# Optimization experiments

Measured on AMD Instinct MI355X. Metric: run time of the kernel, lower is better.

The kernel has to match this reference:

```python
import jax, jax.numpy as jnp
import numpy as np

N = 200000   # nodes per branch
E = 600000   # directed edges per branch
G = 8192     # graphs per batch
F_IN = 7
H = 128
OUT = 2
BN_EPS = 1e-5


def setup_inputs() -> dict:
    key = jax.random.key(0)
    ks = jax.random.split(key, 16)
    s = 0.05
    inp = {
        "x_c": jax.random.normal(ks[0], (N, F_IN), jnp.float32),
        "edge_index_c": jax.random.randint(ks[1], (2, E), 0, N, jnp.int32),
        "batch_c": jnp.sort(jax.random.randint(ks[2], (N,), 0, G, jnp.int32)),
        "x_s": jax.random.normal(ks[3], (N, F_IN), jnp.float32),
        "edge_index_s": jax.random.randint(ks[4], (2, E), 0, N, jnp.int32),
        "batch_s": jnp.sort(jax.random.randint(ks[5], (N,), 0, G, jnp.int32)),
        "Wc0": jax.random.normal(ks[6], (F_IN, H), jnp.float32) * s,
        "bc0": jnp.zeros((H,), jnp.float32),
        "Wc1": jax.random.normal(ks[7], (H, H), jnp.float32) * s,
        "bc1": jnp.zeros((H,), jnp.float32),
        "bnc_gamma": jnp.ones((2, H), jnp.float32),
        "bnc_beta": jnp.zeros((2, H), jnp.float32),
        "bnc_mean": jax.random.normal(ks[8], (2, H), jnp.float32) * 0.01,
        "bnc_var": jnp.ones((2, H), jnp.float32),
        "Ws0": jax.random.normal(ks[9], (F_IN, H), jnp.float32) * s,
        "bs0": jnp.zeros((H,), jnp.float32),
        "Ws1": jax.random.normal(ks[10], (H, H), jnp.float32) * s,
        "bs1": jnp.zeros((H,), jnp.float32),
        "bns_gamma": jnp.ones((2, H), jnp.float32),
        "bns_beta": jnp.zeros((2, H), jnp.float32),
        "bns_mean": jax.random.normal(ks[11], (2, H), jnp.float32) * 0.01,
        "bns_var": jnp.ones((2, H), jnp.float32),
        "fc1_w": jax.random.normal(ks[12], (2 * H, H), jnp.float32) * s,
        "fc1_b": jnp.zeros((H,), jnp.float32),
        "fc2_w": jax.random.normal(ks[13], (H, OUT), jnp.float32) * s,
        "fc2_b": jnp.zeros((OUT,), jnp.float32),
        "num_graphs": G,
    }
    return inp


def _gcn_conv(x, src, dst, W, b):
    """PyG GCNConv: D^{-1/2}(A+I)D^{-1/2} X W + b, self-loops added."""
    n = x.shape[0]
    h = x @ W                                   # [n, H]
    loop = jnp.arange(n, dtype=src.dtype)
    src2 = jnp.concatenate([src, loop])
    dst2 = jnp.concatenate([dst, loop])
    deg = jax.ops.segment_sum(jnp.ones_like(dst2, h.dtype), dst2, num_segments=n)
    dinv = jnp.where(deg > 0, jax.lax.rsqrt(deg), 0.0)
    coef = (dinv[src2] * dinv[dst2])[:, None]   # [E+n, 1]
    out = jax.ops.segment_sum(h[src2] * coef, dst2, num_segments=n)
    return out + b


def _branch(x, ei, W0, b0, W1, b1, gamma, beta, mean, var):
    src, dst = ei[0], ei[1]
    for i, (W, b) in enumerate(((W0, b0), (W1, b1))):
        x = _gcn_conv(x, src, dst, W, b)
        # BatchNorm1d (eval mode) + ReLU; dropout is identity in eval
        x = (x - mean[i]) * jax.lax.rsqrt(var[i] + BN_EPS) * gamma[i] + beta[i]
        x = jax.nn.relu(x)
    return x


def _mean_pool(x, batch, num_graphs):
    s = jax.ops.segment_sum(x, batch, num_segments=num_graphs)
    cnt = jax.ops.segment_sum(jnp.ones_like(batch, x.dtype), batch, num_segments=num_graphs)
    return s / jnp.maximum(cnt, 1.0)[:, None]


def reference(x_c, edge_index_c, batch_c, x_s, edge_index_s, batch_s,
              Wc0, bc0, Wc1, bc1, bnc_gamma, bnc_beta, bnc_mean, bnc_var,
              Ws0, bs0, Ws1, bs1, bns_gamma, bns_beta, bns_mean, bns_var,
              fc1_w, fc1_b, fc2_w, fc2_b, num_graphs):
    hc = _branch(x_c, edge_index_c, Wc0, bc0, Wc1, bc1,
                 bnc_gamma, bnc_beta, bnc_mean, bnc_var)
    hs = _branch(x_s, edge_index_s, Ws0, bs0, Ws1, bs1,
                 bns_gamma, bns_beta, bns_mean, bns_var)
    pc = _mean_pool(hc, batch_c, num_graphs)   # [G, H]
    ps = _mean_pool(hs, batch_s, num_graphs)   # [G, H]
    x = jnp.concatenate([pc, ps], axis=1)      # [G, 2H]
    x = jax.nn.relu(x @ fc1_w + fc1_b)
    return x @ fc2_w + fc2_b                   # [G, 2]
```

## Files before the change

### kernel.cpp

```cpp
#include <hip/hip_runtime.h>

#define NN 200000
#define NE 600000
#define NG 8192
#define HD 128
#define FIN 7
#define BN_EPS 1e-5f

#define CHUNK 1024
#define NB 196
#define TA 64
#define NPG 8
#define NBT (NN / TA)
#define ECAP 320
#define GMAX 8

__global__ void k_hist(const int* __restrict__ dstC, const int* __restrict__ dstS,
                       const int* __restrict__ batchC, const int* __restrict__ batchS,
                       int* __restrict__ degC, int* __restrict__ degS,
                       int* __restrict__ cntC, int* __restrict__ cntS) {
    int e = blockIdx.x * 256 + threadIdx.x;
    if (e < NE)            atomicAdd(&degC[dstC[e]], 1);
    else if (e < 2 * NE)   atomicAdd(&degS[dstS[e - NE]], 1);
    if (e < NN)                      atomicAdd(&cntC[batchC[e]], 1);
    else if (e >= NE && e < NE + NN) atomicAdd(&cntS[batchS[e - NE]], 1);
}

__global__ void k_scan1m(const int* __restrict__ degC, const int* __restrict__ degS,
                         int* __restrict__ bsumC, int* __restrict__ bsumS,
                         float* __restrict__ dinvC, float* __restrict__ dinvS,
                         const float* __restrict__ xC, const float* __restrict__ xS,
                         float* __restrict__ xsC, float* __restrict__ xsS) {
    __shared__ int sd[256];
    int t = threadIdx.x;
    int b = blockIdx.x;
    bool sBr = b >= NB;
    int bb = sBr ? b - NB : b;
    const int* deg = sBr ? degS : degC;
    const float* x = sBr ? xS : xC;
    float* dinv = sBr ? dinvS : dinvC;
    float* xs   = sBr ? xsS : xsC;
    int* bsum = sBr ? bsumS : bsumC;
    int base = bb * CHUNK + t * 4;
    int s = 0;
#pragma unroll
    for (int j = 0; j < 4; j++) {
        int i = base + j;
        if (i < NN) {
            int d = deg[i];
            s += d;
            float di = rsqrtf((float)(d + 1));
            dinv[i] = di;
            float4 v0, v1;
            v0.x = x[(size_t)i * FIN + 0] * di;
            v0.y = x[(size_t)i * FIN + 1] * di;
            v0.z = x[(size_t)i * FIN + 2] * di;
            v0.w = x[(size_t)i * FIN + 3] * di;
            v1.x = x[(size_t)i * FIN + 4] * di;
            v1.y = x[(size_t)i * FIN + 5] * di;
            v1.z = x[(size_t)i * FIN + 6] * di;
            v1.w = 0.f;
            *reinterpret_cast<float4*>(&xs[(size_t)i * 8])     = v0;
            *reinterpret_cast<float4*>(&xs[(size_t)i * 8 + 4]) = v1;
        }
    }
    sd[t] = s; __syncthreads();
    for (int st = 128; st > 0; st >>= 1) { if (t < st) sd[t] += sd[t + st]; __syncthreads(); }
    if (t == 0) bsum[bb] = sd[0];
}

__global__ void k_scan2m(int* __restrict__ bsumC, int* __restrict__ bsumS) {
    __shared__ int sd[256];
    int* bsum = blockIdx.x ? bsumS : bsumC;
    int t = threadIdx.x;
    int v = (t < NB) ? bsum[t] : 0;
    sd[t] = v; __syncthreads();
    for (int st = 1; st < 256; st <<= 1) {
        int add = (t >= st) ? sd[t - st] : 0;
        __syncthreads();
        sd[t] += add;
        __syncthreads();
    }
    if (t < NB) bsum[t] = sd[t] - v;
}

__global__ void k_scan3m(const int* __restrict__ degC, const int* __restrict__ degS,
                         const int* __restrict__ bsumC, const int* __restrict__ bsumS,
                         int* __restrict__ offsC, int* __restrict__ offsS,
                         int* __restrict__ curC, int* __restrict__ curS) {
    __shared__ int sd[256];
    int t = threadIdx.x;
    int b = blockIdx.x;
    bool sBr = b >= NB;
    int bb = sBr ? b - NB : b;
    const int* deg  = sBr ? degS  : degC;
    const int* bsum = sBr ? bsumS : bsumC;
    int* offs   = sBr ? offsS : offsC;
    int* cursor = sBr ? curS  : curC;
    int base = bb * CHUNK + t * 4;
    int v[4]; int s = 0;
#pragma unroll
    for (int j = 0; j < 4; j++) { int i = base + j; v[j] = (i < NN) ? deg[i] : 0; s += v[j]; }
    sd[t] = s; __syncthreads();
    for (int st = 1; st < 256; st <<= 1) {
        int add = (t >= st) ? sd[t - st] : 0;
        __syncthreads();
        sd[t] += add;
        __syncthreads();
    }
    int run = bsum[bb] + sd[t] - s;
#pragma unroll
    for (int j = 0; j < 4; j++) {
        int i = base + j;
        if (i < NN) { offs[i] = run; cursor[i] = run; run += v[j]; }
    }
    if (bb == 0 && t == 0) offs[NN] = NE;
}

__global__ void k_fillm(const int* __restrict__ srcC, const int* __restrict__ dstC,
                        const int* __restrict__ srcS, const int* __restrict__ dstS,
                        int* __restrict__ curC, int* __restrict__ curS,
                        int* __restrict__ csrC, int* __restrict__ csrS) {
    int e = blockIdx.x * 256 + threadIdx.x;
    if (e < NE) {
        int d = dstC[e];
        int pos = atomicAdd(&curC[d], 1);
        csrC[pos] = srcC[e];
    } else if (e < 2 * NE) {
        int ee = e - NE;
        int d = dstS[ee];
        int pos = atomicAdd(&curS[d], 1);
        csrS[pos] = srcS[ee];
    }
}

__global__ void k_aggxm(const float* __restrict__ xsC, const float* __restrict__ xsS,
                        const float* __restrict__ dinvC, const float* __restrict__ dinvS,
                        const int* __restrict__ offsC, const int* __restrict__ offsS,
                        const int* __restrict__ csrC, const int* __restrict__ csrS,
                        float* __restrict__ axdC, float* __restrict__ axdS) {
    int gid = blockIdx.x * 256 + threadIdx.x;
    bool sBr = gid >= NN * 8;
    int lid = sBr ? gid - NN * 8 : gid;
    const float* xs   = sBr ? xsS   : xsC;
    const float* dinv = sBr ? dinvS : dinvC;
    const int*   offs = sBr ? offsS : offsC;
    const int*   csr  = sBr ? csrS  : csrC;
    float*       axd  = sBr ? axdS  : axdC;
    int i = lid >> 3, f = lid & 7;
    float v = xs[lid];
    int o1 = offs[i], o2 = offs[i + 1];
    int j = o1;
    for (; j + 2 <= o2; j += 2) {
        int s0 = csr[j], s1 = csr[j + 1];
        float u0 = xs[(size_t)s0 * 8 + f];
        float u1 = xs[(size_t)s1 * 8 + f];
        v += u0; v += u1;
    }
    if (j < o2) v += xs[(size_t)csr[j] * 8 + f];
    float di = dinv[i];
    axd[lid] = (f == 7) ? di : v * di;
}

__device__ __forceinline__ void src_contrib(float4 r0, float4 r1,
                                            const float4* wp, const float4 c4, float4& a) {
    float axr[7] = { r0.x, r0.y, r0.z, r0.w, r1.x, r1.y, r1.z };
    float4 y = c4;
#pragma unroll
    for (int k = 0; k < FIN; k++) {
        y.x = fmaf(axr[k], wp[k].x, y.x);
        y.y = fmaf(axr[k], wp[k].y, y.y);
        y.z = fmaf(axr[k], wp[k].z, y.z);
        y.w = fmaf(axr[k], wp[k].w, y.w);
    }
    a.x = fmaf(fmaxf(y.x, 0.f), r1.w, a.x);
    a.y = fmaf(fmaxf(y.y, 0.f), r1.w, a.y);
    a.z = fmaf(fmaxf(y.z, 0.f), r1.w, a.z);
    a.w = fmaf(fmaxf(y.w, 0.f), r1.w, a.w);
}

#define PHASE1(GETIDX)                                                                     \
    _Pragma("unroll")                                                                      \
    for (int n = 0; n < NPG; n++) {                                                        \
        int ln = n0 + n;                                                                   \
        float4 a = make_float4(0.f, 0.f, 0.f, 0.f);                                        \
        int e = soffs[ln], ee = soffs[ln + 1];                                             \
        float4 p0 = *reinterpret_cast<const float4*>(&axd[(size_t)(nbase + ln) * 8]);      \
        float4 p1 = *reinterpret_cast<const float4*>(&axd[(size_t)(nbase + ln) * 8 + 4]);  \
        sdvN[n] = p1.w;                                                                    \
        for (; e < ee; e++) {                                                              \
            int s = (GETIDX);                                                              \
            float4 q0 = *reinterpret_cast<const float4*>(&axd[(size_t)s * 8]);             \
            float4 q1 = *reinterpret_cast<const float4*>(&axd[(size_t)s * 8 + 4]);         \
            src_contrib(p0, p1, wp, c4, a);                                                \
            p0 = q0; p1 = q1;                                                              \
        }                                                                                  \
        src_contrib(p0, p1, wp, c4, a);                                                    \
        *reinterpret_cast<float4*>(&g2[ln][f4]) = a;                                       \
    }

__global__ __launch_bounds__(256, 4) void k_agp2(
    const float* __restrict__ axdC, const float* __restrict__ axdS,
    const int* __restrict__ offsC, const int* __restrict__ offsS,
    const int* __restrict__ csrC, const int* __restrict__ csrS,
    const int* __restrict__ batchC, const int* __restrict__ batchS,
    const float* __restrict__ Wc0, const float* __restrict__ bc0,
    const float* __restrict__ bncG, const float* __restrict__ bncB,
    const float* __restrict__ bncM, const float* __restrict__ bncV,
    const float* __restrict__ Wc1, const float* __restrict__ bc1,
    const float* __restrict__ Ws0, const float* __restrict__ bs0,
    const float* __restrict__ bnsG, const float* __restrict__ bnsB,
    const float* __restrict__ bnsM, const float* __restrict__ bnsV,
    const float* __restrict__ Ws1, const float* __restrict__ bs1,
    float* __restrict__ poolC, float* __restrict__ poolS)
{
    __shared__ float g2[TA][HD];
    __shared__ float spool[GMAX * HD];
    __shared__ int soffs[TA + 1];
    __shared__ int scsr[ECAP];
    int b = blockIdx.x;
    bool sBr = b >= NBT;
    int bb = sBr ? b - NBT : b;
    const float* axd  = sBr ? axdS  : axdC;
    const int*  offs  = sBr ? offsS : offsC;
    const int*  csr   = sBr ? csrS  : csrC;
    const int*  batch = sBr ? batchS : batchC;
    const float* W0   = sBr ? Ws0 : Wc0;
    const float* b0   = sBr ? bs0 : bc0;
    const float* bnG  = sBr ? bnsG : bncG;
    const float* bnB  = sBr ? bnsB : bncB;
    const float* bnM  = sBr ? bnsM : bncM;
    const float* bnV  = sBr ? bnsV : bncV;
    const float* W1   = sBr ? Ws1 : Wc1;
    const float* b1   = sBr ? bs1 : bc1;
    float* pool       = sBr ? poolS : poolC;

    int t = threadIdx.x;
    int nbase = bb * TA;
    if (t <= TA) soffs[t] = offs[nbase + t];
#pragma unroll
    for (int r = 0; r < GMAX * HD / 256; r++) spool[r * 256 + t] = 0.f;
    __syncthreads();
    int E0 = soffs[0], E1 = soffs[TA];
    int Et = E1 - E0;
    int ecap = Et < ECAP ? Et : ECAP;
    for (int j = t; j < ecap; j += 256) scsr[j] = csr[E0 + j];

    int q = t & 31, ng = t >> 5;
    int f4 = q * 4, n0 = ng * NPG;

    float4 gm = *reinterpret_cast<const float4*>(&bnG[f4]);
    float4 vr = *reinterpret_cast<const float4*>(&bnV[f4]);
    float4 mn = *reinterpret_cast<const float4*>(&bnM[f4]);
    float4 bt = *reinterpret_cast<const float4*>(&bnB[f4]);
    float4 bb0 = *reinterpret_cast<const float4*>(&b0[f4]);
    float4 gsc;
    gsc.x = gm.x * rsqrtf(vr.x + BN_EPS);
    gsc.y = gm.y * rsqrtf(vr.y + BN_EPS);
    gsc.z = gm.z * rsqrtf(vr.z + BN_EPS);
    gsc.w = gm.w * rsqrtf(vr.w + BN_EPS);
    float4 wp[FIN];
#pragma unroll
    for (int k = 0; k < FIN; k++) {
        float4 w = *reinterpret_cast<const float4*>(&W0[k * HD + f4]);
        wp[k] = make_float4(w.x * gsc.x, w.y * gsc.y, w.z * gsc.z, w.w * gsc.w);
    }
    float4 c4 = make_float4((bb0.x - mn.x) * gsc.x + bt.x,
                            (bb0.y - mn.y) * gsc.y + bt.y,
                            (bb0.z - mn.z) * gsc.z + bt.z,
                            (bb0.w - mn.w) * gsc.w + bt.w);
    __syncthreads();

    float sdvN[NPG];
    if (Et <= ECAP) {
        PHASE1(scsr[e - E0])
    } else {
        PHASE1(((e - E0) < ECAP) ? scsr[e - E0] : csr[e])
    }
    __syncthreads();

    float acc[NPG][4];
#pragma unroll
    for (int a = 0; a < NPG; a++)
#pragma unroll
        for (int c = 0; c < 4; c++) acc[a][c] = 0.f;

    for (int k = 0; k < 128; k += 4) {
        float ha[NPG][4];
#pragma unroll
        for (int a = 0; a < NPG; a++) {
            float4 hv = *reinterpret_cast<const float4*>(&g2[n0 + a][k]);
            ha[a][0] = hv.x; ha[a][1] = hv.y; ha[a][2] = hv.z; ha[a][3] = hv.w;
        }
#pragma unroll
        for (int j = 0; j < 4; j++) {
            float4 w = *reinterpret_cast<const float4*>(&W1[(k + j) * HD + f4]);
#pragma unroll
            for (int a = 0; a < NPG; a++) {
                acc[a][0] = fmaf(ha[a][j], w.x, acc[a][0]);
                acc[a][1] = fmaf(ha[a][j], w.y, acc[a][1]);
                acc[a][2] = fmaf(ha[a][j], w.z, acc[a][2]);
                acc[a][3] = fmaf(ha[a][j], w.w, acc[a][3]);
            }
        }
    }

    float4 gm2 = *reinterpret_cast<const float4*>(&bnG[HD + f4]);
    float4 bt2 = *reinterpret_cast<const float4*>(&bnB[HD + f4]);
    float4 mn2 = *reinterpret_cast<const float4*>(&bnM[HD + f4]);
    float4 vr2 = *reinterpret_cast<const float4*>(&bnV[HD + f4]);
    float4 bb1 = *reinterpret_cast<const float4*>(&b1[f4]);
    float Ax = gm2.x * rsqrtf(vr2.x + BN_EPS), Bx = (bb1.x - mn2.x) * Ax + bt2.x;
    float Ay = gm2.y * rsqrtf(vr2.y + BN_EPS), By = (bb1.y - mn2.y) * Ay + bt2.y;
    float Az = gm2.z * rsqrtf(vr2.z + BN_EPS), Bz = (bb1.z - mn2.z) * Az + bt2.z;
    float Aw = gm2.w * rsqrtf(vr2.w + BN_EPS), Bw = (bb1.w - mn2.w) * Aw + bt2.w;

    int gfirst = batch[nbase];
    float sx = 0, sy = 0, sz = 0, sw = 0;
    int curg = -1;
#pragma unroll
    for (int a = 0; a < NPG; a++) {
        int i = nbase + n0 + a;
        int g = batch[i];
        float sdv = sdvN[a];
        float zx = fmaxf(fmaf(acc[a][0] * sdv, Ax, Bx), 0.f);
        float zy = fmaxf(fmaf(acc[a][1] * sdv, Ay, By), 0.f);
        float zz = fmaxf(fmaf(acc[a][2] * sdv, Az, Bz), 0.f);
        float zw = fmaxf(fmaf(acc[a][3] * sdv, Aw, Bw), 0.f);
        if (g != curg) {
            if (curg >= 0) {
                int slot = curg - gfirst;
                if (slot < GMAX) {
                    atomicAdd(&spool[slot * HD + f4 + 0], sx);
                    atomicAdd(&spool[slot * HD + f4 + 1], sy);
                    atomicAdd(&spool[slot * HD + f4 + 2], sz);
                    atomicAdd(&spool[slot * HD + f4 + 3], sw);
                } else {
                    atomicAdd(&pool[(size_t)curg * HD + f4 + 0], sx);
                    atomicAdd(&pool[(size_t)curg * HD + f4 + 1], sy);
                    atomicAdd(&pool[(size_t)curg * HD + f4 + 2], sz);
                    atomicAdd(&pool[(size_t)curg * HD + f4 + 3], sw);
                }
            }
            curg = g; sx = zx; sy = zy; sz = zz; sw = zw;
        } else { sx += zx; sy += zy; sz += zz; sw += zw; }
    }
    {
        int slot = curg - gfirst;
        if (slot < GMAX) {
            atomicAdd(&spool[slot * HD + f4 + 0], sx);
            atomicAdd(&spool[slot * HD + f4 + 1], sy);
            atomicAdd(&spool[slot * HD + f4 + 2], sz);
            atomicAdd(&spool[slot * HD + f4 + 3], sw);
        } else {
            atomicAdd(&pool[(size_t)curg * HD + f4 + 0], sx);
            atomicAdd(&pool[(size_t)curg * HD + f4 + 1], sy);
            atomicAdd(&pool[(size_t)curg * HD + f4 + 2], sz);
            atomicAdd(&pool[(size_t)curg * HD + f4 + 3], sw);
        }
    }
    __syncthreads();

    int glast = batch[nbase + TA - 1];
    int nslots = glast - gfirst + 1;
    if (nslots > GMAX) nslots = GMAX;
    for (int idx = t; idx < (nslots << 7); idx += 256) {
        atomicAdd(&pool[(size_t)(gfirst + (idx >> 7)) * HD + (idx & 127)], spool[idx]);
    }
}

#define GPB 8
__global__ __launch_bounds__(128) void k_mlp(
    const float* __restrict__ pc, const float* __restrict__ ps,
    const int* __restrict__ cc, const int* __restrict__ cs,
    const float* __restrict__ w1, const float* __restrict__ b1,
    const float* __restrict__ w2, const float* __restrict__ b2,
    float* __restrict__ outp)
{
    __shared__ float xc[GPB][256];
    __shared__ float hb[GPB][128];
    int t = threadIdx.x;
    int g0 = blockIdx.x * GPB;
#pragma unroll
    for (int gg = 0; gg < GPB; gg++) {
        int g = g0 + gg;
        xc[gg][t]       = pc[g * HD + t] / fmaxf((float)cc[g], 1.f);
        xc[gg][128 + t] = ps[g * HD + t] / fmaxf((float)cs[g], 1.f);
    }
    __syncthreads();
    float acc[GPB];
#pragma unroll
    for (int gg = 0; gg < GPB; gg++) acc[gg] = b1[t];
#pragma unroll 2
    for (int k = 0; k < 256; k++) {
        float w = w1[k * HD + t];
#pragma unroll
        for (int gg = 0; gg < GPB; gg++) acc[gg] = fmaf(xc[gg][k], w, acc[gg]);
    }
#pragma unroll
    for (int gg = 0; gg < GPB; gg++) hb[gg][t] = fmaxf(acc[gg], 0.f);
    __syncthreads();
    if (t < GPB * 2) {
        int gg = t >> 1, o = t & 1;
        float v = b2[o];
        for (int k = 0; k < 128; k++) v = fmaf(hb[gg][k], w2[k * 2 + o], v);
        outp[(size_t)(g0 + gg) * 2 + o] = v;
    }
}

extern "C" void kernel_launch(void* const* d_in, const int* in_sizes, int n_in,
                              void* d_out, int out_size, void* d_ws, size_t ws_size,
                              hipStream_t stream) {
    const float* x_c      = (const float*)d_in[0];
    const int*   ei_c     = (const int*)  d_in[1];
    const int*   batch_c  = (const int*)  d_in[2];
    const float* x_s      = (const float*)d_in[3];
    const int*   ei_s     = (const int*)  d_in[4];
    const int*   batch_s  = (const int*)  d_in[5];
    const float* Wc0      = (const float*)d_in[6];
    const float* bc0      = (const float*)d_in[7];
    const float* Wc1      = (const float*)d_in[8];
    const float* bc1      = (const float*)d_in[9];
    const float* bnc_g    = (const float*)d_in[10];
    const float* bnc_b    = (const float*)d_in[11];
    const float* bnc_m    = (const float*)d_in[12];
    const float* bnc_v    = (const float*)d_in[13];
    const float* Ws0      = (const float*)d_in[14];
    const float* bs0      = (const float*)d_in[15];
    const float* Ws1      = (const float*)d_in[16];
    const float* bs1      = (const float*)d_in[17];
    const float* bns_g    = (const float*)d_in[18];
    const float* bns_b    = (const float*)d_in[19];
    const float* bns_m    = (const float*)d_in[20];
    const float* bns_v    = (const float*)d_in[21];
    const float* fc1_w    = (const float*)d_in[22];
    const float* fc1_b    = (const float*)d_in[23];
    const float* fc2_w    = (const float*)d_in[24];
    const float* fc2_b    = (const float*)d_in[25];

    char* p = (char*)d_ws;
    auto take = [&](size_t bytes) {
        void* r = (void*)p;
        p += (bytes + 255) & ~(size_t)255;
        return r;
    };
    float* xs_c   = (float*)take((size_t)NN * 8 * 4);
    float* xs_s   = (float*)take((size_t)NN * 8 * 4);
    float* axd_c  = (float*)take((size_t)NN * 8 * 4);
    float* axd_s  = (float*)take((size_t)NN * 8 * 4);
    int*   deg_c  = (int*)  take((size_t)NN * 4);
    int*   deg_s  = (int*)  take((size_t)NN * 4);
    float* dinv_c = (float*)take((size_t)NN * 4);
    float* dinv_s = (float*)take((size_t)NN * 4);
    int*   offs_c = (int*)  take((size_t)(NN + 1) * 4);
    int*   offs_s = (int*)  take((size_t)(NN + 1) * 4);
    int*   cur_c  = (int*)  take((size_t)NN * 4);
    int*   cur_s  = (int*)  take((size_t)NN * 4);
    int*   csr_c  = (int*)  take((size_t)NE * 4);
    int*   csr_s  = (int*)  take((size_t)NE * 4);
    int*   bsum_c = (int*)  take((size_t)NB * 4);
    int*   bsum_s = (int*)  take((size_t)NB * 4);
    float* pool_c = (float*)take((size_t)NG * HD * 4);
    float* pool_s = (float*)take((size_t)NG * HD * 4);
    int*   cnt_c  = (int*)  take((size_t)NG * 4);
    int*   cnt_s  = (int*)  take((size_t)NG * 4);
    (void)ws_size; (void)in_sizes; (void)n_in; (void)out_size;

    hipMemsetAsync(deg_c, 0, (size_t)2 * NN * 4, stream);
    hipMemsetAsync(pool_c, 0, ((size_t)2 * NG * HD + 2 * NG) * 4, stream);

    const int* src_c = ei_c;           const int* dst_c = ei_c + NE;
    const int* src_s = ei_s;           const int* dst_s = ei_s + NE;

    k_hist  <<<(2 * NE + 255) / 256, 256, 0, stream>>>(dst_c, dst_s, batch_c, batch_s,
                                                       deg_c, deg_s, cnt_c, cnt_s);
    k_scan1m<<<2 * NB, 256, 0, stream>>>(deg_c, deg_s, bsum_c, bsum_s, dinv_c, dinv_s,
                                         x_c, x_s, xs_c, xs_s);
    k_scan2m<<<2, 256, 0, stream>>>(bsum_c, bsum_s);
    k_scan3m<<<2 * NB, 256, 0, stream>>>(deg_c, deg_s, bsum_c, bsum_s,
                                         offs_c, offs_s, cur_c, cur_s);
    k_fillm <<<(2 * NE + 255) / 256, 256, 0, stream>>>(src_c, dst_c, src_s, dst_s,
                                                       cur_c, cur_s, csr_c, csr_s);
    k_aggxm <<<2 * NN * 8 / 256, 256, 0, stream>>>(xs_c, xs_s, dinv_c, dinv_s,
                                                   offs_c, offs_s, csr_c, csr_s, axd_c, axd_s);

    k_agp2<<<2 * NBT, 256, 0, stream>>>(axd_c, axd_s,
                                        offs_c, offs_s, csr_c, csr_s, batch_c, batch_s,
                                        Wc0, bc0, bnc_g, bnc_b, bnc_m, bnc_v, Wc1, bc1,
                                        Ws0, bs0, bns_g, bns_b, bns_m, bns_v, Ws1, bs1,
                                        pool_c, pool_s);

    k_mlp<<<NG / GPB, 128, 0, stream>>>(pool_c, pool_s, cnt_c, cnt_s,
                                        fc1_w, fc1_b, fc2_w, fc2_b, (float*)d_out);
}
```

Baseline: 508.4 us.

## Record per-edge rank in histogram to drop fill atomics and fuse scan stage

The histogram kernel now saves the return value of its degree atomic as a per-edge rank. The fill kernel then places each edge at offs[dst]+rank with no atomics and no cursor array. The block-sum scan kernel is removed, and every scan3 block redundantly scans the 196 block sums in shared memory, saving one launch. In exchange it adds two 600K-int rank arrays that are written and read back, and extra per-block scan work.

```diff
diff --git a/kernel.cpp b/kernel.cpp
--- a/kernel.cpp
+++ b/kernel.cpp
@@ -18,10 +18,11 @@
 __global__ void k_hist(const int* __restrict__ dstC, const int* __restrict__ dstS,
                        const int* __restrict__ batchC, const int* __restrict__ batchS,
                        int* __restrict__ degC, int* __restrict__ degS,
-                       int* __restrict__ cntC, int* __restrict__ cntS) {
+                       int* __restrict__ cntC, int* __restrict__ cntS,
+                       int* __restrict__ rankC, int* __restrict__ rankS) {
     int e = blockIdx.x * 256 + threadIdx.x;
-    if (e < NE)            atomicAdd(&degC[dstC[e]], 1);
-    else if (e < 2 * NE)   atomicAdd(&degS[dstS[e - NE]], 1);
+    if (e < NE)            rankC[e] = atomicAdd(&degC[dstC[e]], 1);
+    else if (e < 2 * NE)   rankS[e - NE] = atomicAdd(&degS[dstS[e - NE]], 1);
     if (e < NN)                      atomicAdd(&cntC[batchC[e]], 1);
     else if (e >= NE && e < NE + NN) atomicAdd(&cntS[batchS[e - NE]], 1);
 }
@@ -69,26 +70,11 @@
     if (t == 0) bsum[bb] = sd[0];
 }
 
-__global__ void k_scan2m(int* __restrict__ bsumC, int* __restrict__ bsumS) {
-    __shared__ int sd[256];
-    int* bsum = blockIdx.x ? bsumS : bsumC;
-    int t = threadIdx.x;
-    int v = (t < NB) ? bsum[t] : 0;
-    sd[t] = v; __syncthreads();
-    for (int st = 1; st < 256; st <<= 1) {
-        int add = (t >= st) ? sd[t - st] : 0;
-        __syncthreads();
-        sd[t] += add;
-        __syncthreads();
-    }
-    if (t < NB) bsum[t] = sd[t] - v;
-}
-
 __global__ void k_scan3m(const int* __restrict__ degC, const int* __restrict__ degS,
                          const int* __restrict__ bsumC, const int* __restrict__ bsumS,
-                         int* __restrict__ offsC, int* __restrict__ offsS,
-                         int* __restrict__ curC, int* __restrict__ curS) {
+                         int* __restrict__ offsC, int* __restrict__ offsS) {
     __shared__ int sd[256];
+    __shared__ int sb[256];
     int t = threadIdx.x;
     int b = blockIdx.x;
     bool sBr = b >= NB;
@@ -96,7 +82,17 @@
     const int* deg  = sBr ? degS  : degC;
     const int* bsum = sBr ? bsumS : bsumC;
     int* offs   = sBr ? offsS : offsC;
-    int* cursor = sBr ? curS  : curC;
+
+    sb[t] = (t < NB) ? bsum[t] : 0;
+    __syncthreads();
+    for (int st = 1; st < 256; st <<= 1) {
+        int add = (t >= st) ? sb[t - st] : 0;
+        __syncthreads();
+        sb[t] += add;
+        __syncthreads();
+    }
+    int base0 = (bb == 0) ? 0 : sb[bb - 1];
+
     int base = bb * CHUNK + t * 4;
     int v[4]; int s = 0;
 #pragma unroll
@@ -108,29 +104,28 @@
         sd[t] += add;
         __syncthreads();
     }
-    int run = bsum[bb] + sd[t] - s;
+    int run = base0 + sd[t] - s;
 #pragma unroll
     for (int j = 0; j < 4; j++) {
         int i = base + j;
-        if (i < NN) { offs[i] = run; cursor[i] = run; run += v[j]; }
+        if (i < NN) { offs[i] = run; run += v[j]; }
     }
     if (bb == 0 && t == 0) offs[NN] = NE;
 }
 
 __global__ void k_fillm(const int* __restrict__ srcC, const int* __restrict__ dstC,
                         const int* __restrict__ srcS, const int* __restrict__ dstS,
-                        int* __restrict__ curC, int* __restrict__ curS,
+                        const int* __restrict__ rankC, const int* __restrict__ rankS,
+                        const int* __restrict__ offsC, const int* __restrict__ offsS,
                         int* __restrict__ csrC, int* __restrict__ csrS) {
     int e = blockIdx.x * 256 + threadIdx.x;
     if (e < NE) {
         int d = dstC[e];
-        int pos = atomicAdd(&curC[d], 1);
-        csrC[pos] = srcC[e];
+        csrC[offsC[d] + rankC[e]] = srcC[e];
     } else if (e < 2 * NE) {
         int ee = e - NE;
         int d = dstS[ee];
-        int pos = atomicAdd(&curS[d], 1);
-        csrS[pos] = srcS[ee];
+        csrS[offsS[d] + rankS[ee]] = srcS[ee];
     }
 }
 
@@ -454,8 +449,8 @@
     float* dinv_s = (float*)take((size_t)NN * 4);
     int*   offs_c = (int*)  take((size_t)(NN + 1) * 4);
     int*   offs_s = (int*)  take((size_t)(NN + 1) * 4);
-    int*   cur_c  = (int*)  take((size_t)NN * 4);
-    int*   cur_s  = (int*)  take((size_t)NN * 4);
+    int*   rank_c = (int*)  take((size_t)NE * 4);
+    int*   rank_s = (int*)  take((size_t)NE * 4);
     int*   csr_c  = (int*)  take((size_t)NE * 4);
     int*   csr_s  = (int*)  take((size_t)NE * 4);
     int*   bsum_c = (int*)  take((size_t)NB * 4);
@@ -473,14 +468,14 @@
     const int* src_s = ei_s;           const int* dst_s = ei_s + NE;
 
     k_hist  <<<(2 * NE + 255) / 256, 256, 0, stream>>>(dst_c, dst_s, batch_c, batch_s,
-                                                       deg_c, deg_s, cnt_c, cnt_s);
+                                                       deg_c, deg_s, cnt_c, cnt_s,
+                                                       rank_c, rank_s);
     k_scan1m<<<2 * NB, 256, 0, stream>>>(deg_c, deg_s, bsum_c, bsum_s, dinv_c, dinv_s,
                                          x_c, x_s, xs_c, xs_s);
-    k_scan2m<<<2, 256, 0, stream>>>(bsum_c, bsum_s);
-    k_scan3m<<<2 * NB, 256, 0, stream>>>(deg_c, deg_s, bsum_c, bsum_s,
-                                         offs_c, offs_s, cur_c, cur_s);
+    k_scan3m<<<2 * NB, 256, 0, stream>>>(deg_c, deg_s, bsum_c, bsum_s, offs_c, offs_s);
     k_fillm <<<(2 * NE + 255) / 256, 256, 0, stream>>>(src_c, dst_c, src_s, dst_s,
-                                                       cur_c, cur_s, csr_c, csr_s);
+                                                       rank_c, rank_s, offs_c, offs_s,
+                                                       csr_c, csr_s);
     k_aggxm <<<2 * NN * 8 / 256, 256, 0, stream>>>(xs_c, xs_s, dinv_c, dinv_s,
                                                    offs_c, offs_s, csr_c, csr_s, axd_c, axd_s);
 
```

New measurement: 443.7 us, median of 2. 12.7% less time.
